# Kernel tuning notes

Measured on AMD Instinct MI355X. Metric: run time of the kernel, lower is better.

Reference implementation:

```python
import jax, jax.numpy as jnp
import numpy as np

N = 50000   # nodes per graph
E = 400000  # edges per graph (avg degree 8)
L = 16      # regex token length per edge
V = 64      # VOCAB_SIZE
EMB = 32    # REGEX_EMBEDDING_DIMENSION
H = 128     # LSTM_DIMENSION
D = 373     # hidden_vector_dim (MAX_STATES=50)
IN_IDX = 161
OUT_IDX = 320
SID = 53    # MAX_STATES + 3
SLOPE = 0.2 # GATv2 leaky_relu negative slope

def _lstm_cell(x_t, h, c, Wih, Whh, b):
    g = x_t @ Wih.T + h @ Whh.T + b          # [E, 4H], torch gate order i,f,g,o
    i, f, gg, o = jnp.split(g, 4, axis=-1)
    c = jax.nn.sigmoid(f) * c + jax.nn.sigmoid(i) * jnp.tanh(gg)
    h = jax.nn.sigmoid(o) * jnp.tanh(c)
    return h, c

def _edge_scalar(tokens, embed, Wih_f, Whh_f, b_f, Wih_r, Whh_r, b_r, W1, b1, W2, b2):
    emb = embed.at[0].set(0.0)[tokens]       # padding_idx=0; [E, L, EMB]
    En = tokens.shape[0]
    h0 = jnp.zeros((En, H), jnp.float32)
    def step(carry, x_t):
        h, c = _lstm_cell(x_t, carry[0], carry[1], Wih_f, Whh_f, b_f)
        return (h, c), None
    (h_fwd, _), _ = jax.lax.scan(step, (h0, h0), jnp.swapaxes(emb, 0, 1))
    # bidirectional output at last timestep: reverse direction has consumed only token L-1
    h_bwd, _ = _lstm_cell(emb[:, -1], h0, h0, Wih_r, Whh_r, b_r)
    feat = jax.nn.relu(jnp.concatenate([h_fwd, h_bwd], axis=-1) @ W1 + b1)
    return jax.nn.relu(feat @ W2 + b2)[:, 0]  # [E]

def _gatv2(x, src, dst, Wl, bl, Wr, br, att, bias):
    xl = x @ Wl + bl                          # source transform (messages)
    xr = x @ Wr + br                          # target transform
    m = jax.nn.leaky_relu(xl[src] + xr[dst], SLOPE)  # [E, D]
    e = m @ att                                      # [E]
    e_max = jax.ops.segment_max(e, dst, num_segments=N)
    ex = jnp.exp(e - e_max[dst])
    denom = jax.ops.segment_sum(ex, dst, num_segments=N)
    alpha = ex / (denom[dst] + 1e-16)                # scatter-softmax over in-edges
    agg = jax.ops.segment_sum(alpha[:, None] * xl[src], dst, num_segments=N)
    return agg + bias

def _process(x, ei, edge_attr, Wl, bl, Wr, br, att, bias):
    src, dst = ei[0], ei[1]
    src_id = jnp.argmax(x[src, :SID], axis=-1)
    tgt_id = jnp.argmax(x[dst, :SID], axis=-1)
    x = x.at[dst, IN_IDX + src_id].set(edge_attr)   # index_put scatter writes
    x = x.at[src, OUT_IDX + tgt_id].set(edge_attr)
    return jax.nn.relu(_gatv2(x, src, dst, Wl, bl, Wr, br, att, bias) + x)

def setup_inputs():
    key = jax.random.key(0)
    ks = jax.random.split(key, 40)
    rn = lambda k, s, sc=0.05: jax.random.normal(k, s, dtype=jnp.float32) * sc
    return {
        "fx": jax.random.normal(ks[0], (N, D), dtype=jnp.float32),
        "bx": jax.random.normal(ks[1], (N, D), dtype=jnp.float32),
        "f_edge_index": jax.random.randint(ks[2], (2, E), 0, N),
        "b_edge_index": jax.random.randint(ks[3], (2, E), 0, N),
        "f_tokens": jax.random.randint(ks[4], (E, L), 0, V),
        "b_tokens": jax.random.randint(ks[5], (E, L), 0, V),
        "embed": rn(ks[6], (V, EMB), 1.0),
        "Wih_f": rn(ks[7], (4 * H, EMB)),
        "Whh_f": rn(ks[8], (4 * H, H)),
        "bih_f": rn(ks[9], (4 * H,)),
        "bhh_f": rn(ks[10], (4 * H,)),
        "Wih_r": rn(ks[11], (4 * H, EMB)),
        "Whh_r": rn(ks[12], (4 * H, H)),
        "bih_r": rn(ks[13], (4 * H,)),
        "bhh_r": rn(ks[14], (4 * H,)),
        "W1": rn(ks[15], (2 * H, 32)),
        "b1": rn(ks[16], (32,)),
        "W2": rn(ks[17], (32, 1)),
        "b2": rn(ks[18], (1,)),
        "fWl": rn(ks[19], (D, D)), "fbl": rn(ks[20], (D,)),
        "fWr": rn(ks[21], (D, D)), "fbr": rn(ks[22], (D,)),
        "fatt": rn(ks[23], (D,)), "fbias": rn(ks[24], (D,)),
        "bWl": rn(ks[25], (D, D)), "bbl": rn(ks[26], (D,)),
        "bWr": rn(ks[27], (D, D)), "bbr": rn(ks[28], (D,)),
        "batt": rn(ks[29], (D,)), "bbias": rn(ks[30], (D,)),
    }

def reference(fx, bx, f_edge_index, b_edge_index, f_tokens, b_tokens, embed,
              Wih_f, Whh_f, bih_f, bhh_f, Wih_r, Whh_r, bih_r, bhh_r,
              W1, b1, W2, b2,
              fWl, fbl, fWr, fbr, fatt, fbias,
              bWl, bbl, bWr, bbr, batt, bbias):
    b_f = bih_f + bhh_f
    b_r = bih_r + bhh_r
    f_ea = _edge_scalar(f_tokens, embed, Wih_f, Whh_f, b_f, Wih_r, Whh_r, b_r, W1, b1, W2, b2)
    b_ea = _edge_scalar(b_tokens, embed, Wih_f, Whh_f, b_f, Wih_r, Whh_r, b_r, W1, b1, W2, b2)
    fxo = _process(fx, f_edge_index, f_ea, fWl, fbl, fWr, fbr, fatt, fbias)
    bxo = _process(bx, b_edge_index, b_ea, bWl, bbl, bWr, bbr, batt, bbias)
    return jnp.concatenate([fxo, bxo], axis=-1)  # [N, 2*D]
```

## Files before the change

kernel.cpp:

```cpp
#include <hip/hip_runtime.h>
#include <cstdint>


#define D_DIM   373
#define SID_N   53
#define IN_COL  161
#define OUT_COL 320
#define HS_STRIDE 136
#define EDGES_T 32
#define N_ES    2

typedef short bf16x8 __attribute__((ext_vector_type(8)));
typedef float f32x4  __attribute__((ext_vector_type(4)));

#define LOG2E_F 1.4426950408889634f
#define TWO_LOG2E_F 2.8853900817779268f

__device__ __forceinline__ float fast_exp2(float x) {
#if __has_builtin(__builtin_amdgcn_exp2f)
  return __builtin_amdgcn_exp2f(x);
#else
  return exp2f(x);
#endif
}
__device__ __forceinline__ float fast_rcp(float x) {
#if __has_builtin(__builtin_amdgcn_rcpf)
  return __builtin_amdgcn_rcpf(x);
#else
  return 1.0f / x;
#endif
}
__device__ __forceinline__ float sig_ref(float x)  { return 1.0f / (1.0f + __expf(-x)); }
__device__ __forceinline__ float tanh_ref(float x) { return 2.0f / (1.0f + __expf(-2.0f * x)) - 1.0f; }

__device__ __forceinline__ unsigned short f2bf(float f) {
  unsigned u = __float_as_uint(f);
  unsigned r = (u + 0x7fffu + ((u >> 16) & 1u)) >> 16;
  return (unsigned short)r;
}
__device__ __forceinline__ float bflo2f(unsigned u) { return __uint_as_float(u << 16); }
__device__ __forceinline__ float bfhi2f(unsigned u) { return __uint_as_float(u & 0xffff0000u); }
__device__ __forceinline__ unsigned cvt_pk_bf16(float lo, float hi) {
  unsigned r;
  asm("v_cvt_pk_bf16_f32 %0, %1, %2" : "=v"(r) : "v"(lo), "v"(hi));
  return r;
}
__device__ __forceinline__ float pair_sig_tanh(float A, float B) {
  return (B - 1.0f) * fast_rcp((1.0f + A) * (1.0f + B));
}

__global__ void fill_u32_kernel(unsigned* __restrict__ p, unsigned v, size_t n) {
  size_t i = (size_t)blockIdx.x * blockDim.x + threadIdx.x;
  size_t stride = (size_t)gridDim.x * blockDim.x;
  for (; i < n; i += stride) p[i] = v;
}

__global__ void precompute_kernel(
    const float* __restrict__ embed, const float* __restrict__ Wih_f,
    const float* __restrict__ Whh_f,
    const float* __restrict__ bih_f, const float* __restrict__ bhh_f,
    const float* __restrict__ Wih_r,
    const float* __restrict__ bih_r, const float* __restrict__ bhh_r,
    const float* __restrict__ W1, const float* __restrict__ b1,
    unsigned short* __restrict__ Pg, unsigned short* __restrict__ BfragW,
    unsigned short* __restrict__ Bfrag1, float* __restrict__ FB)
{
  __shared__ float ps[512];
  __shared__ float gb[512];
  __shared__ float hb[128];
  int v = blockIdx.x;
  int j = threadIdx.x;

  float s = 0.0f;
  if (v != 0) {
    #pragma unroll
    for (int k = 0; k < 32; ++k) s += embed[v * 32 + k] * Wih_f[j * 32 + k];
  }
  ps[j] = s + bih_f[j] + bhh_f[j];

  float gr = bih_r[j] + bhh_r[j];
  if (v != 0) {
    #pragma unroll
    for (int k = 0; k < 32; ++k) gr += embed[v * 32 + k] * Wih_r[j * 32 + k];
  }
  gb[j] = gr;
  __syncthreads();
  if (j < 128) {
    float c = sig_ref(gb[j]) * tanh_ref(gb[256 + j]);
    hb[j] = sig_ref(gb[384 + j]) * tanh_ref(c);
  }
  __syncthreads();

  { int h = j >> 2, g = j & 3;
    float sc = (g == 2) ? TWO_LOG2E_F : -LOG2E_F;
    Pg[((size_t)v * 128 + h) * 4 + g] = f2bf(ps[g * 128 + h] * sc); }

  if (j < 32) {
    float s2 = b1[j];
    for (int m = 0; m < 128; ++m) s2 += hb[m] * W1[(128 + m) * 32 + j];
    FB[v * 32 + j] = s2;
  }

  if (v == 0) {
    for (int f = j; f < 65536; f += 512) {
      int e = f & 7, l = (f >> 3) & 63, ks = (f >> 9) & 3, nt = f >> 11;
      int n = nt * 16 + (l & 15);
      int k = ks * 32 + (l >> 4) * 8 + e;
      float sc = ((nt >> 3) == 2) ? TWO_LOG2E_F : -LOG2E_F;
      BfragW[f] = f2bf(Whh_f[(size_t)n * 128 + k] * sc);
    }
  }
  if (v == 1) {
    for (int f = j; f < 4096; f += 512) {
      int e = f & 7, l = (f >> 3) & 63, ks = (f >> 9) & 3, n2 = f >> 11;
      int q = n2 * 16 + (l & 15);
      int k = ks * 32 + (l >> 4) * 8 + e;
      Bfrag1[f] = f2bf(W1[(size_t)k * 32 + q]);
    }
  }
}

__global__ __launch_bounds__(512, 4) void lstm_mfma_kernel(
    const int*   __restrict__ tokens,
    const unsigned short* __restrict__ Pg,
    const unsigned short* __restrict__ BfragW,
    const unsigned short* __restrict__ Bfrag1,
    const float* __restrict__ FB,
    const float* __restrict__ W2,
    const float* __restrict__ b2,
    float* __restrict__ ea, int E, int nTiles)
{
  __shared__ unsigned short Hs[2][EDGES_T * HS_STRIDE];
  __shared__ int toks[16][EDGES_T];

  int tid  = threadIdx.x;
  int lane = tid & 63;
  int wv2  = tid >> 6;
  int l15  = lane & 15;
  int lg   = lane >> 4;
  int hbase = wv2 * 16 + lg * 4;

  bf16x8 BW[4][4];
  #pragma unroll
  for (int gate = 0; gate < 4; ++gate)
    #pragma unroll
    for (int ks = 0; ks < 4; ++ks)
      BW[gate][ks] = *(const bf16x8*)(BfragW +
          ((size_t)((gate * 8 + wv2) * 4 + ks) * 64 + lane) * 8);
  float4 w2lo = *(const float4*)(W2 + lg * 4);
  float4 w2hi = *(const float4*)(W2 + 16 + lg * 4);
  float b2v = b2[0];

  for (int tile = blockIdx.x; tile < nTiles; tile += gridDim.x) {
    int e0 = tile * EDGES_T;
    if (tid < 16 * EDGES_T) {
      int m = tid >> 4, t = tid & 15;
      int ee = e0 + m; if (ee >= E) ee = E - 1;
      toks[t][m] = tokens[(size_t)ee * 16 + t];
    }
    __syncthreads();

    f32x4 cst[N_ES];
    #pragma unroll
    for (int es = 0; es < N_ES; ++es) {
      int eL = es * 16 + l15;
      unsigned po4 = (unsigned)(toks[0][eL] * 128 + hbase) * 4u;
      const uint4* pp = (const uint4*)(Pg + po4);
      uint4 pa = pp[0], pb = pp[1];
      float pi[4] = {bflo2f(pa.x), bflo2f(pa.z), bflo2f(pb.x), bflo2f(pb.z)};
      float pg[4] = {bflo2f(pa.y), bflo2f(pa.w), bflo2f(pb.y), bflo2f(pb.w)};
      float po[4] = {bfhi2f(pa.y), bfhi2f(pa.w), bfhi2f(pb.y), bfhi2f(pb.w)};
      float h[4];
      #pragma unroll
      for (int r = 0; r < 4; ++r) {
        float A = fast_exp2(pi[r]);
        float B = fast_exp2(pg[r]);
        float O = fast_exp2(po[r]);
        float cn = pair_sig_tanh(A, B);
        cst[es][r] = cn;
        float C = fast_exp2(TWO_LOG2E_F * cn);
        h[r] = pair_sig_tanh(O, C);
      }
      uint2 hp = make_uint2(cvt_pk_bf16(h[0], h[1]), cvt_pk_bf16(h[2], h[3]));
      *(uint2*)(&Hs[0][eL * HS_STRIDE + hbase]) = hp;
    }
    __syncthreads();

    int cur = 0;
    #pragma unroll 1
    for (int t = 1; t < 16; ++t) {
      #pragma unroll
      for (int es = 0; es < N_ES; ++es) {
        int eL = es * 16 + l15;
        unsigned po4 = (unsigned)(toks[t][eL] * 128 + hbase) * 4u;
        const uint4* pp = (const uint4*)(Pg + po4);
        uint4 pa = pp[0], pb = pp[1];
        f32x4 acc[4];
        acc[0] = (f32x4){bflo2f(pa.x), bflo2f(pa.z), bflo2f(pb.x), bflo2f(pb.z)};
        acc[1] = (f32x4){bfhi2f(pa.x), bfhi2f(pa.z), bfhi2f(pb.x), bfhi2f(pb.z)};
        acc[2] = (f32x4){bflo2f(pa.y), bflo2f(pa.w), bflo2f(pb.y), bflo2f(pb.w)};
        acc[3] = (f32x4){bfhi2f(pa.y), bfhi2f(pa.w), bfhi2f(pb.y), bfhi2f(pb.w)};

        #pragma unroll
        for (int ks = 0; ks < 4; ++ks) {
          bf16x8 Hf = *(const bf16x8*)(&Hs[cur][eL * HS_STRIDE + ks * 32 + lg * 8]);
          #pragma unroll
          for (int gate = 0; gate < 4; ++gate)
            acc[gate] = __builtin_amdgcn_mfma_f32_16x16x32_bf16(
                BW[gate][ks], Hf, acc[gate], 0, 0, 0);
        }

        float h[4];
        #pragma unroll
        for (int r = 0; r < 4; ++r) {
          float A = fast_exp2(acc[0][r]);
          float F = fast_exp2(acc[1][r]);
          float B = fast_exp2(acc[2][r]);
          float O = fast_exp2(acc[3][r]);
          float ig = pair_sig_tanh(A, B);
          float f  = fast_rcp(1.0f + F);
          float cn = fmaf(f, cst[es][r], ig);
          cst[es][r] = cn;
          float C = fast_exp2(TWO_LOG2E_F * cn);
          h[r] = pair_sig_tanh(O, C);
        }
        uint2 hp = make_uint2(cvt_pk_bf16(h[0], h[1]), cvt_pk_bf16(h[2], h[3]));
        *(uint2*)(&Hs[cur ^ 1][eL * HS_STRIDE + hbase]) = hp;
      }
      cur ^= 1;
      __syncthreads();
    }

    if (wv2 < N_ES) {
      int eL = wv2 * 16 + l15;
      bf16x8 Hf[4];
      #pragma unroll
      for (int ks = 0; ks < 4; ++ks)
        Hf[ks] = *(const bf16x8*)(&Hs[cur][eL * HS_STRIDE + ks * 32 + lg * 8]);
      f32x4 a2[2];
      a2[0] = (f32x4){0.f, 0.f, 0.f, 0.f};
      a2[1] = (f32x4){0.f, 0.f, 0.f, 0.f};
      #pragma unroll
      for (int ks = 0; ks < 4; ++ks)
        #pragma unroll
        for (int n2 = 0; n2 < 2; ++n2)
          a2[n2] = __builtin_amdgcn_mfma_f32_16x16x32_bf16(
              *(const bf16x8*)(Bfrag1 + ((size_t)(n2 * 4 + ks) * 64 + lane) * 8),
              Hf[ks], a2[n2], 0, 0, 0);
      int v15 = toks[15][eL];
      float4 fb0 = *(const float4*)(FB + v15 * 32 + lg * 4);
      float4 fb1 = *(const float4*)(FB + v15 * 32 + 16 + lg * 4);
      float pr = fmaxf(a2[0][0] + fb0.x, 0.f) * w2lo.x
               + fmaxf(a2[0][1] + fb0.y, 0.f) * w2lo.y
               + fmaxf(a2[0][2] + fb0.z, 0.f) * w2lo.z
               + fmaxf(a2[0][3] + fb0.w, 0.f) * w2lo.w
               + fmaxf(a2[1][0] + fb1.x, 0.f) * w2hi.x
               + fmaxf(a2[1][1] + fb1.y, 0.f) * w2hi.y
               + fmaxf(a2[1][2] + fb1.z, 0.f) * w2hi.z
               + fmaxf(a2[1][3] + fb1.w, 0.f) * w2hi.w;
      pr += __shfl_xor(pr, 16);
      pr += __shfl_xor(pr, 32);
      int eidx = e0 + eL;
      if (lane < 16 && eidx < E) ea[eidx] = fmaxf(pr + b2v, 0.0f);
    }
    __syncthreads();
  }
}

__global__ void argmax_winner_kernel(
    const float* __restrict__ x, const int* __restrict__ ei, int E,
    int* __restrict__ srcid, int* __restrict__ tgtid,
    int* __restrict__ win_in, int* __restrict__ win_out)
{
  int e = blockIdx.x * 256 + threadIdx.x;
  if (e >= E) return;
  int s = ei[e];
  int t = ei[E + e];
  const float* xs = x + (size_t)s * D_DIM;
  int sid = 0; float bv = xs[0];
  for (int k = 1; k < SID_N; ++k) { float v = xs[k]; if (v > bv) { bv = v; sid = k; } }
  const float* xt = x + (size_t)t * D_DIM;
  int tix = 0; bv = xt[0];
  for (int k = 1; k < SID_N; ++k) { float v = xt[k]; if (v > bv) { bv = v; tix = k; } }
  srcid[e] = sid;
  tgtid[e] = tix;
  atomicMax(&win_in[(size_t)t * SID_N + sid], e);
  atomicMax(&win_out[(size_t)s * SID_N + tix], e);
}

__global__ void scatter_resolve_kernel(
    const int* __restrict__ ei, const float* __restrict__ ea,
    const int* __restrict__ srcid, const int* __restrict__ tgtid,
    const int* __restrict__ win_in, const int* __restrict__ win_out,
    float* __restrict__ x_mod, int E)
{
  int e = blockIdx.x * 256 + threadIdx.x;
  if (e >= E) return;
  int s = ei[e];
  int t = ei[E + e];
  int sid = srcid[e], tix = tgtid[e];
  if (win_in[(size_t)t * SID_N + sid] == e)
    x_mod[(size_t)t * D_DIM + IN_COL + sid] = ea[e];
  if (win_out[(size_t)s * SID_N + tix] == e)
    x_mod[(size_t)s * D_DIM + OUT_COL + tix] = ea[e];
}

__global__ void pack_w_kernel(const float* __restrict__ Wl,
                              const float* __restrict__ Wr,
                              unsigned short* __restrict__ Wfrag)
{
  int f = blockIdx.x * 256 + threadIdx.x;
  if (f >= 48 * 12 * 64 * 8) return;
  int e = f & 7, l = (f >> 3) & 63;
  int rest = f >> 9;
  int ks = rest % 12, nt = rest / 12;
  int nl = nt * 16 + (l & 15);
  int k  = ks * 32 + (l >> 4) * 8 + e;
  float val = 0.0f;
  if (k < D_DIM) {
    if (nl < D_DIM)                      val = Wl[(size_t)k * D_DIM + nl];
    else if (nl >= 384 && nl < 384 + D_DIM) val = Wr[(size_t)k * D_DIM + (nl - 384)];
  }
  Wfrag[f] = f2bf(val);
}

__global__ __launch_bounds__(256, 2) void gemm_mfma_kernel(
    const float* __restrict__ A,
    const unsigned short* __restrict__ Wfrag,
    const float* __restrict__ bl, const float* __restrict__ br,
    float* __restrict__ xl, float* __restrict__ xr, int N)
{
  __shared__ unsigned short As[64][40];
  int tid  = threadIdx.x;
  int lane = tid & 63;
  int wv   = tid >> 6;
  int l15  = lane & 15, lg = lane >> 4;
  int m0   = blockIdx.x * 64;
  int nt   = blockIdx.y * 4 + wv;

  f32x4 acc[4];
  #pragma unroll
  for (int i = 0; i < 4; ++i) acc[i] = (f32x4){0.f, 0.f, 0.f, 0.f};

  int srow = tid >> 2, seg = tid & 3;
  int gr = m0 + srow; if (gr >= N) gr = N - 1;
  const float* arow = A + (size_t)gr * D_DIM;

  for (int ks = 0; ks < 12; ++ks) {
    int c0 = ks * 32 + seg * 8;
    float v[8];
    #pragma unroll
    for (int j = 0; j < 8; ++j) v[j] = (c0 + j < D_DIM) ? arow[c0 + j] : 0.0f;
    unsigned pk0 = cvt_pk_bf16(v[0], v[1]);
    unsigned pk1 = cvt_pk_bf16(v[2], v[3]);
    unsigned pk2 = cvt_pk_bf16(v[4], v[5]);
    unsigned pk3 = cvt_pk_bf16(v[6], v[7]);
    __syncthreads();
    *(uint4*)(&As[srow][seg * 8]) = make_uint4(pk0, pk1, pk2, pk3);
    __syncthreads();

    bf16x8 Bf = *(const bf16x8*)(Wfrag + ((size_t)(nt * 12 + ks) * 64 + lane) * 8);
    #pragma unroll
    for (int msub = 0; msub < 4; ++msub) {
      bf16x8 Af = *(const bf16x8*)(&As[msub * 16 + l15][lg * 8]);
      acc[msub] = __builtin_amdgcn_mfma_f32_16x16x32_bf16(Af, Bf, acc[msub], 0, 0, 0);
    }
  }

  int nl = nt * 16 + l15;
  float* dst = nullptr; int col = 0; const float* bias_ = nullptr;
  if (nl < D_DIM)                         { dst = xl; col = nl;       bias_ = bl; }
  else if (nl >= 384 && nl < 384 + D_DIM) { dst = xr; col = nl - 384; bias_ = br; }
  if (dst) {
    float bv = bias_[col];
    #pragma unroll
    for (int msub = 0; msub < 4; ++msub) {
      #pragma unroll
      for (int r = 0; r < 4; ++r) {
        int m = m0 + msub * 16 + lg * 4 + r;
        if (m < N) dst[(size_t)m * D_DIM + col] = acc[msub][r] + bv;
      }
    }
  }
}

__global__ __launch_bounds__(256) void edge_e_kernel(
    const float* __restrict__ xl, const float* __restrict__ xr,
    const float* __restrict__ att, const int* __restrict__ ei,
    float* __restrict__ e_buf, int E)
{
  int widx = (blockIdx.x * 256 + threadIdx.x) >> 6;
  int lane = threadIdx.x & 63;
  if (widx >= E) return;
  int s = ei[widx], t = ei[E + widx];
  const float* pl = xl + (size_t)s * D_DIM;
  const float* pr = xr + (size_t)t * D_DIM;
  float acc = 0.0f;
  for (int d = lane; d < D_DIM; d += 64) {
    float m = pl[d] + pr[d];
    m = (m > 0.0f) ? m : 0.2f * m;
    acc += m * att[d];
  }
  #pragma unroll
  for (int o = 32; o > 0; o >>= 1) acc += __shfl_down(acc, o);
  if (lane == 0) e_buf[widx] = acc;
}

__global__ void hist_kernel(const int* __restrict__ ei, unsigned* __restrict__ deg,
                            int E) {
  int e = blockIdx.x * 256 + threadIdx.x;
  if (e >= E) return;
  atomicAdd(&deg[ei[E + e]], 1u);
}

__global__ void scan1_kernel(const unsigned* __restrict__ deg,
                             unsigned* __restrict__ excl,
                             unsigned* __restrict__ bsum, int n) {
  __shared__ unsigned s[256];
  int t = threadIdx.x;
  int i = blockIdx.x * 256 + t;
  unsigned v = (i < n) ? deg[i] : 0u;
  s[t] = v; __syncthreads();
  #pragma unroll
  for (int o = 1; o < 256; o <<= 1) {
    unsigned u = (t >= o) ? s[t - o] : 0u;
    __syncthreads();
    s[t] += u;
    __syncthreads();
  }
  if (i < n) excl[i] = s[t] - v;
  if (t == 255) bsum[blockIdx.x] = s[255];
}

__global__ void scan2_kernel(unsigned* __restrict__ bsum, int nb) {
  __shared__ unsigned s[256];
  int t = threadIdx.x;
  unsigned v = (t < nb) ? bsum[t] : 0u;
  s[t] = v; __syncthreads();
  #pragma unroll
  for (int o = 1; o < 256; o <<= 1) {
    unsigned u = (t >= o) ? s[t - o] : 0u;
    __syncthreads();
    s[t] += u;
    __syncthreads();
  }
  if (t < nb) bsum[t] = s[t] - v;
}

__global__ void scan3_kernel(unsigned* __restrict__ excl,
                             const unsigned* __restrict__ bsum, int n) {
  int i = blockIdx.x * 256 + threadIdx.x;
  if (i < n) excl[i] += bsum[i >> 8];
}

__global__ void place_kernel(const int* __restrict__ ei,
                             unsigned* __restrict__ offs,
                             int* __restrict__ csr_eid, int E) {
  int e = blockIdx.x * 256 + threadIdx.x;
  if (e >= E) return;
  unsigned j = atomicAdd(&offs[ei[E + e]], 1u);
  csr_eid[j] = e;
}

__global__ __launch_bounds__(256) void node_gat_kernel(
    const int* __restrict__ ei, const int* __restrict__ csr_eid,
    const unsigned* __restrict__ offs, const unsigned* __restrict__ deg,
    float* __restrict__ ebuf, const float* __restrict__ xl,
    const float* __restrict__ xmod, const float* __restrict__ bias,
    float* __restrict__ out, int N, int E, int goff)
{
  int n = (blockIdx.x * 256 + threadIdx.x) >> 6;
  int lane = threadIdx.x & 63;
  if (n >= N) return;
  unsigned end = offs[n], d = deg[n], start = end - d;

  float mx = -3.4e38f;
  for (unsigned j = start; j < end; ++j)
    mx = fmaxf(mx, ebuf[csr_eid[j]]);
  float den = 0.0f;
  for (unsigned j = start; j < end; ++j) {
    int eid = csr_eid[j];
    float ex = __expf(ebuf[eid] - mx);
    ebuf[eid] = ex;
    den += ex;
  }
  float inv = 1.0f / (den + 1e-16f);

  float o0 = 0, o1 = 0, o2 = 0, o3 = 0, o4 = 0, o5 = 0;
  for (unsigned j = start; j < end; ++j) {
    int eid = csr_eid[j];
    float w = ebuf[eid] * inv;
    const float* row = xl + (size_t)ei[eid] * D_DIM;
    o0 = fmaf(w, row[lane], o0);
    o1 = fmaf(w, row[64 + lane], o1);
    o2 = fmaf(w, row[128 + lane], o2);
    o3 = fmaf(w, row[192 + lane], o3);
    o4 = fmaf(w, row[256 + lane], o4);
    if (lane < 53) o5 = fmaf(w, row[320 + lane], o5);
  }

  const float* xm = xmod + (size_t)n * D_DIM;
  float* op = out + (size_t)n * (2 * D_DIM) + goff;
  op[lane]       = fmaxf(o0 + bias[lane]       + xm[lane],       0.0f);
  op[64 + lane]  = fmaxf(o1 + bias[64 + lane]  + xm[64 + lane],  0.0f);
  op[128 + lane] = fmaxf(o2 + bias[128 + lane] + xm[128 + lane], 0.0f);
  op[192 + lane] = fmaxf(o3 + bias[192 + lane] + xm[192 + lane], 0.0f);
  op[256 + lane] = fmaxf(o4 + bias[256 + lane] + xm[256 + lane], 0.0f);
  if (lane < 53)
    op[320 + lane] = fmaxf(o5 + bias[320 + lane] + xm[320 + lane], 0.0f);
}

extern "C" void kernel_launch(void* const* d_in, const int* in_sizes, int n_in,
                              void* d_out, int out_size, void* d_ws, size_t ws_size,
                              hipStream_t stream)
{
  const float* fx     = (const float*)d_in[0];
  const float* bx     = (const float*)d_in[1];
  const int*   fei    = (const int*)d_in[2];
  const int*   bei    = (const int*)d_in[3];
  const int*   ftk    = (const int*)d_in[4];
  const int*   btk    = (const int*)d_in[5];
  const float* embed  = (const float*)d_in[6];
  const float* Wih_f  = (const float*)d_in[7];
  const float* Whh_f  = (const float*)d_in[8];
  const float* bih_f  = (const float*)d_in[9];
  const float* bhh_f  = (const float*)d_in[10];
  const float* Wih_r  = (const float*)d_in[11];
  const float* bih_r  = (const float*)d_in[13];
  const float* bhh_r  = (const float*)d_in[14];
  const float* W1     = (const float*)d_in[15];
  const float* b1     = (const float*)d_in[16];
  const float* W2     = (const float*)d_in[17];
  const float* b2     = (const float*)d_in[18];

  const float* Wl_g[2]   = {(const float*)d_in[19], (const float*)d_in[25]};
  const float* bl_g[2]   = {(const float*)d_in[20], (const float*)d_in[26]};
  const float* Wr_g[2]   = {(const float*)d_in[21], (const float*)d_in[27]};
  const float* br_g[2]   = {(const float*)d_in[22], (const float*)d_in[28]};
  const float* att_g[2]  = {(const float*)d_in[23], (const float*)d_in[29]};
  const float* bias_g[2] = {(const float*)d_in[24], (const float*)d_in[30]};
  const float* x_g[2]    = {fx, bx};
  const int*   ei_g[2]   = {fei, bei};
  const int*   tk_g[2]   = {ftk, btk};

  const int E = in_sizes[2] / 2;
  const int N = in_sizes[0] / D_DIM;

  char* wsb = (char*)d_ws;
  size_t off = 0;
  auto alloc = [&](size_t bytes) -> void* {
    void* p = wsb + off; off += (bytes + 255) & ~(size_t)255; return p;
  };
  unsigned short* Pg     = (unsigned short*)alloc((size_t)64 * 128 * 4 * 2);
  unsigned short* BfragW = (unsigned short*)alloc((size_t)65536 * 2);
  unsigned short* Bfrag1 = (unsigned short*)alloc((size_t)4096 * 2);
  unsigned short* Wfrag2 = (unsigned short*)alloc((size_t)2 * 294912 * 2);
  float* FB    = (float*)alloc((size_t)64 * 32 * 4);
  float* ea    = (float*)alloc((size_t)E * 4);
  float* ebuf  = (float*)alloc((size_t)E * 4);
  int*   srcid = (int*)alloc((size_t)E * 4);
  int*   tgtid = (int*)alloc((size_t)E * 4);
  int*   csr_eid = (int*)alloc((size_t)E * 4);
  unsigned* deg  = (unsigned*)alloc((size_t)N * 4);
  unsigned* offs = (unsigned*)alloc((size_t)N * 4);
  unsigned* bsum = (unsigned*)alloc((size_t)256 * 4);
  int* win_in  = (int*)alloc((size_t)N * SID_N * 4);
  int* win_out = (int*)alloc((size_t)N * SID_N * 4);
  float* xmod  = (float*)alloc((size_t)N * D_DIM * 4);
  float* xl    = (float*)alloc((size_t)N * D_DIM * 4);
  float* xr    = (float*)alloc((size_t)N * D_DIM * 4);
  (void)ws_size; (void)n_in; (void)out_size;

  const size_t win_u32 = (size_t)((char*)win_out - (char*)win_in) / 4
                         + (size_t)N * SID_N;

  float* out = (float*)d_out;

  precompute_kernel<<<64, 512, 0, stream>>>(
      embed, Wih_f, Whh_f, bih_f, bhh_f, Wih_r, bih_r, bhh_r, W1, b1,
      Pg, BfragW, Bfrag1, FB);
  pack_w_kernel<<<(294912 + 255) / 256, 256, 0, stream>>>(
      Wl_g[0], Wr_g[0], Wfrag2);
  pack_w_kernel<<<(294912 + 255) / 256, 256, 0, stream>>>(
      Wl_g[1], Wr_g[1], Wfrag2 + 294912);

  const int nTiles  = (E + EDGES_T - 1) / EDGES_T;
  const int gridL   = nTiles < 2048 ? nTiles : 2048;
  const int gridE   = (E + 255) / 256;
  const int gridEW  = (E + 3) / 4;
  const int nScanB  = (N + 255) / 256;
  const int gridNd  = (N * 64 + 255) / 256;
  dim3 gridG((N + 63) / 64, 12);

  for (int g = 0; g < 2; ++g) {
    const float* x  = x_g[g];
    const int*   ei = ei_g[g];

    lstm_mfma_kernel<<<gridL, 512, 0, stream>>>(tk_g[g], Pg, BfragW, Bfrag1,
                                                FB, W2, b2, ea, E, nTiles);

    hipMemcpyAsync(xmod, x, (size_t)N * D_DIM * sizeof(float),
                   hipMemcpyDeviceToDevice, stream);
    fill_u32_kernel<<<2048, 256, 0, stream>>>((unsigned*)win_in, 0xFFFFFFFFu,
                                              win_u32);
    argmax_winner_kernel<<<gridE, 256, 0, stream>>>(x, ei, E, srcid, tgtid,
                                                    win_in, win_out);
    scatter_resolve_kernel<<<gridE, 256, 0, stream>>>(ei, ea, srcid, tgtid,
                                                      win_in, win_out, xmod, E);

    gemm_mfma_kernel<<<gridG, 256, 0, stream>>>(xmod, Wfrag2 + (size_t)g * 294912,
                                                bl_g[g], br_g[g], xl, xr, N);

    fill_u32_kernel<<<512, 256, 0, stream>>>(deg, 0u, (size_t)N);
    hist_kernel<<<gridE, 256, 0, stream>>>(ei, deg, E);
    scan1_kernel<<<nScanB, 256, 0, stream>>>(deg, offs, bsum, N);
    scan2_kernel<<<1, 256, 0, stream>>>(bsum, nScanB);
    scan3_kernel<<<nScanB, 256, 0, stream>>>(offs, bsum, N);
    place_kernel<<<gridE, 256, 0, stream>>>(ei, offs, csr_eid, E);

    edge_e_kernel<<<gridEW, 256, 0, stream>>>(xl, xr, att_g[g], ei, ebuf, E);
    node_gat_kernel<<<gridNd, 256, 0, stream>>>(ei, csr_eid, offs, deg, ebuf,
                                                xl, xmod, bias_g[g], out,
                                                N, E, g * D_DIM);
  }
}
```

Before: 3.744 ms.

## Double LSTM edge tile and store input-gate table in fp32 gate-major layout

Measured after the change: 4.667 ms. 1.25x slower.

```diff
diff --git a/kernel.cpp b/kernel.cpp
--- a/kernel.cpp
+++ b/kernel.cpp
@@ -7,8 +7,8 @@
 #define IN_COL  161
 #define OUT_COL 320
 #define HS_STRIDE 136
-#define EDGES_T 32
-#define N_ES    2
+#define EDGES_T 64
+#define N_ES    4
 
 typedef short bf16x8 __attribute__((ext_vector_type(8)));
 typedef float f32x4  __attribute__((ext_vector_type(4)));
@@ -38,8 +38,6 @@
   unsigned r = (u + 0x7fffu + ((u >> 16) & 1u)) >> 16;
   return (unsigned short)r;
 }
-__device__ __forceinline__ float bflo2f(unsigned u) { return __uint_as_float(u << 16); }
-__device__ __forceinline__ float bfhi2f(unsigned u) { return __uint_as_float(u & 0xffff0000u); }
 __device__ __forceinline__ unsigned cvt_pk_bf16(float lo, float hi) {
   unsigned r;
   asm("v_cvt_pk_bf16_f32 %0, %1, %2" : "=v"(r) : "v"(lo), "v"(hi));
@@ -62,10 +60,9 @@
     const float* __restrict__ Wih_r,
     const float* __restrict__ bih_r, const float* __restrict__ bhh_r,
     const float* __restrict__ W1, const float* __restrict__ b1,
-    unsigned short* __restrict__ Pg, unsigned short* __restrict__ BfragW,
+    float* __restrict__ Pg32, unsigned short* __restrict__ BfragW,
     unsigned short* __restrict__ Bfrag1, float* __restrict__ FB)
 {
-  __shared__ float ps[512];
   __shared__ float gb[512];
   __shared__ float hb[128];
   int v = blockIdx.x;
@@ -76,7 +73,7 @@
     #pragma unroll
     for (int k = 0; k < 32; ++k) s += embed[v * 32 + k] * Wih_f[j * 32 + k];
   }
-  ps[j] = s + bih_f[j] + bhh_f[j];
+  s += bih_f[j] + bhh_f[j];
 
   float gr = bih_r[j] + bhh_r[j];
   if (v != 0) {
@@ -91,9 +88,9 @@
   }
   __syncthreads();
 
-  { int h = j >> 2, g = j & 3;
-    float sc = (g == 2) ? TWO_LOG2E_F : -LOG2E_F;
-    Pg[((size_t)v * 128 + h) * 4 + g] = f2bf(ps[g * 128 + h] * sc); }
+  { int gate = j >> 7;
+    float sc = (gate == 2) ? TWO_LOG2E_F : -LOG2E_F;
+    Pg32[(size_t)v * 512 + j] = s * sc; }
 
   if (j < 32) {
     float s2 = b1[j];
@@ -120,9 +117,9 @@
   }
 }
 
-__global__ __launch_bounds__(512, 4) void lstm_mfma_kernel(
+__global__ __launch_bounds__(512, 2) void lstm_mfma_kernel(
     const int*   __restrict__ tokens,
-    const unsigned short* __restrict__ Pg,
+    const float* __restrict__ Pg32,
     const unsigned short* __restrict__ BfragW,
     const unsigned short* __restrict__ Bfrag1,
     const float* __restrict__ FB,
@@ -139,6 +136,7 @@
   int l15  = lane & 15;
   int lg   = lane >> 4;
   int hbase = wv2 * 16 + lg * 4;
+  const float* PgL = Pg32 + hbase;
 
   bf16x8 BW[4][4];
   #pragma unroll
@@ -153,8 +151,8 @@
 
   for (int tile = blockIdx.x; tile < nTiles; tile += gridDim.x) {
     int e0 = tile * EDGES_T;
-    if (tid < 16 * EDGES_T) {
-      int m = tid >> 4, t = tid & 15;
+    for (int i = tid; i < 16 * EDGES_T; i += 512) {
+      int m = i >> 4, t = i & 15;
       int ee = e0 + m; if (ee >= E) ee = E - 1;
       toks[t][m] = tokens[(size_t)ee * 16 + t];
     }
@@ -164,18 +162,16 @@
     #pragma unroll
     for (int es = 0; es < N_ES; ++es) {
       int eL = es * 16 + l15;
-      unsigned po4 = (unsigned)(toks[0][eL] * 128 + hbase) * 4u;
-      const uint4* pp = (const uint4*)(Pg + po4);
-      uint4 pa = pp[0], pb = pp[1];
-      float pi[4] = {bflo2f(pa.x), bflo2f(pa.z), bflo2f(pb.x), bflo2f(pb.z)};
-      float pg[4] = {bflo2f(pa.y), bflo2f(pa.w), bflo2f(pb.y), bflo2f(pb.w)};
-      float po[4] = {bfhi2f(pa.y), bfhi2f(pa.w), bfhi2f(pb.y), bfhi2f(pb.w)};
+      const float* pb = PgL + (unsigned)toks[0][eL] * 512u;
+      f32x4 ai = *(const f32x4*)(pb);
+      f32x4 ag = *(const f32x4*)(pb + 256);
+      f32x4 ao = *(const f32x4*)(pb + 384);
       float h[4];
       #pragma unroll
       for (int r = 0; r < 4; ++r) {
-        float A = fast_exp2(pi[r]);
-        float B = fast_exp2(pg[r]);
-        float O = fast_exp2(po[r]);
+        float A = fast_exp2(ai[r]);
+        float B = fast_exp2(ag[r]);
+        float O = fast_exp2(ao[r]);
         float cn = pair_sig_tanh(A, B);
         cst[es][r] = cn;
         float C = fast_exp2(TWO_LOG2E_F * cn);
@@ -192,14 +188,12 @@
       #pragma unroll
       for (int es = 0; es < N_ES; ++es) {
         int eL = es * 16 + l15;
-        unsigned po4 = (unsigned)(toks[t][eL] * 128 + hbase) * 4u;
-        const uint4* pp = (const uint4*)(Pg + po4);
-        uint4 pa = pp[0], pb = pp[1];
+        const float* pb = PgL + (unsigned)toks[t][eL] * 512u;
         f32x4 acc[4];
-        acc[0] = (f32x4){bflo2f(pa.x), bflo2f(pa.z), bflo2f(pb.x), bflo2f(pb.z)};
-        acc[1] = (f32x4){bfhi2f(pa.x), bfhi2f(pa.z), bfhi2f(pb.x), bfhi2f(pb.z)};
-        acc[2] = (f32x4){bflo2f(pa.y), bflo2f(pa.w), bflo2f(pb.y), bflo2f(pb.w)};
-        acc[3] = (f32x4){bfhi2f(pa.y), bfhi2f(pa.w), bfhi2f(pb.y), bfhi2f(pb.w)};
+        acc[0] = *(const f32x4*)(pb);
+        acc[1] = *(const f32x4*)(pb + 128);
+        acc[2] = *(const f32x4*)(pb + 256);
+        acc[3] = *(const f32x4*)(pb + 384);
 
         #pragma unroll
         for (int ks = 0; ks < 4; ++ks) {
@@ -551,7 +545,7 @@
   auto alloc = [&](size_t bytes) -> void* {
     void* p = wsb + off; off += (bytes + 255) & ~(size_t)255; return p;
   };
-  unsigned short* Pg     = (unsigned short*)alloc((size_t)64 * 128 * 4 * 2);
+  float* Pg32            = (float*)alloc((size_t)64 * 512 * 4);
   unsigned short* BfragW = (unsigned short*)alloc((size_t)65536 * 2);
   unsigned short* Bfrag1 = (unsigned short*)alloc((size_t)4096 * 2);
   unsigned short* Wfrag2 = (unsigned short*)alloc((size_t)2 * 294912 * 2);
@@ -578,7 +572,7 @@
 
   precompute_kernel<<<64, 512, 0, stream>>>(
       embed, Wih_f, Whh_f, bih_f, bhh_f, Wih_r, bih_r, bhh_r, W1, b1,
-      Pg, BfragW, Bfrag1, FB);
+      Pg32, BfragW, Bfrag1, FB);
   pack_w_kernel<<<(294912 + 255) / 256, 256, 0, stream>>>(
       Wl_g[0], Wr_g[0], Wfrag2);
   pack_w_kernel<<<(294912 + 255) / 256, 256, 0, stream>>>(
@@ -596,7 +590,7 @@
     const float* x  = x_g[g];
     const int*   ei = ei_g[g];
 
-    lstm_mfma_kernel<<<gridL, 512, 0, stream>>>(tk_g[g], Pg, BfragW, Bfrag1,
+    lstm_mfma_kernel<<<gridL, 512, 0, stream>>>(tk_g[g], Pg32, BfragW, Bfrag1,
                                                 FB, W2, b2, ea, E, nTiles);
 
     hipMemcpyAsync(xmod, x, (size_t)N * D_DIM * sizeof(float),
```
